# Optimization experiments

Hardware: AMD Instinct MI355X
Metric: run time of the kernel (lower is better)

Reference implementation:

```python
import jax, jax.numpy as jnp
import numpy as np

NODE_IN, EDGE_IN, HID, L = 16, 8, 128, 4
N_NODES, N_EDGES = 50000, 600000
EPS = 1e-5


def setup_inputs() -> dict:
    key = jax.random.key(0)
    ks = jax.random.split(key, 20)
    def lin(k, fan_in, fan_out):
        b = 1.0 / np.sqrt(fan_in)
        kw, kb = jax.random.split(k)
        return (jax.random.uniform(kw, (fan_in, fan_out), jnp.float32, -b, b),
                jax.random.uniform(kb, (fan_out,), jnp.float32, -b, b))
    x = jax.random.normal(ks[0], (N_NODES, NODE_IN), jnp.float32)
    edge_index = jax.random.randint(ks[1], (2, N_EDGES), 0, N_NODES, jnp.int64)
    edge_attr = jax.random.normal(ks[2], (N_EDGES, EDGE_IN), jnp.float32)
    node_w, node_b = lin(ks[3], NODE_IN, HID)
    edge_w, edge_b = lin(ks[4], EDGE_IN, HID)
    lnode_w, lnode_b, ledge_w, ledge_b, adm_w, adm_b = [], [], [], [], [], []
    for l in range(L):
        w, b = lin(ks[5 + 3 * l], HID, HID); lnode_w.append(w); lnode_b.append(b)
        w, b = lin(ks[6 + 3 * l], HID, HID); ledge_w.append(w); ledge_b.append(b)
        w, b = lin(ks[7 + 3 * l], HID, 1); adm_w.append(w); adm_b.append(b)
    return {
        "x": x, "edge_index": edge_index, "edge_attr": edge_attr,
        "node_w": node_w, "node_b": node_b, "edge_w": edge_w, "edge_b": edge_b,
        "lnode_w": jnp.stack(lnode_w), "lnode_b": jnp.stack(lnode_b),
        "ledge_w": jnp.stack(ledge_w), "ledge_b": jnp.stack(ledge_b),
        "adm_w": jnp.stack(adm_w), "adm_b": jnp.stack(adm_b),
        "gamma": jnp.ones((L, HID), jnp.float32),
        "beta": jnp.zeros((L, HID), jnp.float32),
    }


def reference(x, edge_index, edge_attr, node_w, node_b, edge_w, edge_b,
              lnode_w, lnode_b, ledge_w, ledge_b, adm_w, adm_b, gamma, beta):
    N = x.shape[0]
    src, dst = edge_index[0], edge_index[1]
    h = x @ node_w + node_b              # [N, HID]
    ea = edge_attr @ edge_w + edge_b     # [E, HID]
    for l in range(lnode_w.shape[0]):
        hn = h @ lnode_w[l] + lnode_b[l]                         # lin_node
        y_mag = jax.nn.sigmoid(ea @ adm_w[l] + adm_b[l])         # [E, 1] admittance gate
        e = ea @ ledge_w[l] + ledge_b[l]                         # lin_edge
        msg = y_mag * (hn[src] + e)                              # gated message [E, HID]
        agg = jax.ops.segment_sum(msg, dst, num_segments=N)      # scatter-add
        mu = jnp.mean(agg, axis=-1, keepdims=True)
        var = jnp.mean((agg - mu) ** 2, axis=-1, keepdims=True)
        xn = (agg - mu) * jax.lax.rsqrt(var + EPS) * gamma[l] + beta[l]
        h = h + jax.nn.relu(xn)          # dropout is identity in eval mode
    return h
```

## Files before the change

### kernel.cpp

```cpp
#include <hip/hip_runtime.h>
#include <math.h>

#define N_NODES 50000
#define N_EDGES 600000
#define HID 128
#define NLAYERS 4
#define NODE_IN 16
#define EDGE_IN 8
#define LN_EPS 1e-5f
#define SCAN_BLOCKS ((N_NODES + 255) / 256)

typedef short bf16x8 __attribute__((ext_vector_type(8)));
typedef float f32x4 __attribute__((ext_vector_type(4)));

__device__ __forceinline__ float b2f(unsigned short u) {
    union { unsigned int i; float f; } v; v.i = ((unsigned int)u) << 16; return v.f;
}
__device__ __forceinline__ unsigned short f2b(float x) {
    union { float f; unsigned int i; } v; v.f = x;
    unsigned int b = v.i + 0x7FFFu + ((v.i >> 16) & 1u);
    return (unsigned short)(b >> 16);
}

__global__ void detect_i64(const int* ei, int* flag) {
    __shared__ int nz;
    if (threadIdx.x == 0) nz = 0;
    __syncthreads();
    int acc = 0;
    for (int i = threadIdx.x; i < 1024; i += blockDim.x)
        if (ei[2 * i + 1] != 0) acc = 1;
    if (acc) atomicOr(&nz, 1);
    __syncthreads();
    if (threadIdx.x == 0) *flag = (nz == 0) ? 1 : 0;
}

__device__ __forceinline__ int edge_src(const void* ei, int f, int e) {
    if (f) return (int)((const long long*)ei)[e];
    return ((const int*)ei)[e];
}
__device__ __forceinline__ int edge_dst(const void* ei, int f, int e) {
    if (f) return (int)((const long long*)ei)[N_EDGES + e];
    return ((const int*)ei)[N_EDGES + e];
}

__global__ void hist_k(const void* ei, const int* flag, int* cursor) {
    int e = blockIdx.x * blockDim.x + threadIdx.x;
    if (e >= N_EDGES) return;
    int f = *flag;
    atomicAdd(&cursor[edge_dst(ei, f, e)], 1);
}

__global__ void scan1_k(const int* __restrict__ cursor, int* __restrict__ locex,
                        int* __restrict__ partials) {
    __shared__ int sd[256];
    int t = threadIdx.x, i = blockIdx.x * 256 + t;
    int v = (i < N_NODES) ? cursor[i] : 0;
    sd[t] = v;
    __syncthreads();
    for (int off = 1; off < 256; off <<= 1) {
        int x = (t >= off) ? sd[t - off] : 0;
        __syncthreads();
        sd[t] += x;
        __syncthreads();
    }
    if (i < N_NODES) locex[i] = sd[t] - v;
    if (t == 255) partials[blockIdx.x] = sd[255];
}

__global__ void scan2_k(int* partials) {
    __shared__ int sd[256];
    int t = threadIdx.x;
    int v = (t < SCAN_BLOCKS) ? partials[t] : 0;
    sd[t] = v;
    __syncthreads();
    for (int off = 1; off < 256; off <<= 1) {
        int x = (t >= off) ? sd[t - off] : 0;
        __syncthreads();
        sd[t] += x;
        __syncthreads();
    }
    if (t < SCAN_BLOCKS) partials[t] = sd[t] - v;
    if (t == 255) partials[SCAN_BLOCKS] = sd[255];
}

__global__ void scan3_k(int* __restrict__ row_ptr, int* __restrict__ cursor,
                        const int* __restrict__ partials) {
    int i = blockIdx.x * 256 + threadIdx.x;
    if (i < N_NODES) {
        int r = row_ptr[i] + partials[blockIdx.x];
        row_ptr[i] = r;
        cursor[i] = r;
    }
    if (i == N_NODES) row_ptr[N_NODES] = partials[SCAN_BLOCKS];
}

__global__ void place_k(const void* ei, const int* flag, int* cursor,
                        int* sorted_src, int* sorted_eid) {
    int e = blockIdx.x * blockDim.x + threadIdx.x;
    if (e >= N_EDGES) return;
    int f = *flag;
    int s = edge_src(ei, f, e);
    int d = edge_dst(ei, f, e);
    int pos = atomicAdd(&cursor[d], 1);
    sorted_src[pos] = s;
    sorted_eid[pos] = e;
}

__global__ void precompute_k(const float* __restrict__ edge_w, const float* __restrict__ edge_b,
                             const float* __restrict__ ledge_w, const float* __restrict__ ledge_b,
                             const float* __restrict__ lnode_b,
                             const float* __restrict__ adm_w, const float* __restrict__ adm_b,
                             float* __restrict__ M, float* __restrict__ cb,
                             float* __restrict__ v, float* __restrict__ cgate) {
    int t = blockIdx.x * 256 + threadIdx.x;
    if (t < 4096) {
        int l = t >> 10, k = (t >> 7) & 7, ch = t & 127;
        const float* lw = ledge_w + (size_t)l * HID * HID;
        float a = 0.f;
        for (int j = 0; j < HID; ++j) a += edge_w[k * HID + j] * lw[j * HID + ch];
        M[t] = a;
    } else if (t < 4608) {
        int u = t - 4096;
        int l = u >> 7, ch = u & 127;
        const float* lw = ledge_w + (size_t)l * HID * HID;
        float a = ledge_b[l * HID + ch] + lnode_b[l * HID + ch];
        for (int j = 0; j < HID; ++j) a += edge_b[j] * lw[j * HID + ch];
        cb[u] = a;
    } else if (t < 4640) {
        int u = t - 4608;
        int l = u >> 3, k = u & 7;
        float a = 0.f;
        for (int j = 0; j < HID; ++j) a += edge_w[k * HID + j] * adm_w[l * HID + j];
        v[u] = a;
    } else if (t < 4644) {
        int l = t - 4640;
        float a = adm_b[l];
        for (int j = 0; j < HID; ++j) a += edge_b[j] * adm_w[l * HID + j];
        cgate[l] = a;
    }
}

__global__ void convertw_k(const float* __restrict__ lnode_w, unsigned short* __restrict__ Wt16) {
    int idx = blockIdx.x * 256 + threadIdx.x;
    if (idx >= NLAYERS * HID * HID) return;
    int l = idx >> 14, r = idx & 16383, n = r >> 7, k = r & 127;
    Wt16[idx] = f2b(lnode_w[(size_t)l * HID * HID + k * HID + n]);
}

__global__ __launch_bounds__(256) void yorig_k(const float* __restrict__ edge_attr,
                                               const float* __restrict__ v,
                                               const float* __restrict__ cgate,
                                               float4* __restrict__ y4) {
    __shared__ float sv[36];
    if (threadIdx.x < 32) sv[threadIdx.x] = v[threadIdx.x];
    else if (threadIdx.x < 36) sv[threadIdx.x] = cgate[threadIdx.x - 32];
    __syncthreads();
    int e = blockIdx.x * 256 + threadIdx.x;
    if (e >= N_EDGES) return;
    float4 a0 = ((const float4*)edge_attr)[(size_t)e * 2];
    float4 a1 = ((const float4*)edge_attr)[(size_t)e * 2 + 1];
    float pr[NLAYERS];
#pragma unroll
    for (int l = 0; l < NLAYERS; ++l) {
        const float* vl = &sv[l * 8];
        float p = sv[32 + l];
        p += a0.x * vl[0] + a0.y * vl[1] + a0.z * vl[2] + a0.w * vl[3];
        p += a1.x * vl[4] + a1.y * vl[5] + a1.z * vl[6] + a1.w * vl[7];
        pr[l] = 1.0f / (1.0f + expf(-p));
    }
    y4[e] = make_float4(pr[0], pr[1], pr[2], pr[3]);
}

__global__ __launch_bounds__(256) void node_stats_k(
    const int* __restrict__ row_ptr, const int* __restrict__ sorted_eid,
    const float* __restrict__ edge_attr, const float4* __restrict__ y4,
    float* __restrict__ agg8, float* __restrict__ sy_arr,
    float* __restrict__ y_sorted) {
    int lane = threadIdx.x & 63;
    int n = (blockIdx.x * 256 + threadIdx.x) >> 6;
    if (n >= N_NODES) return;
    int es = lane >> 3, k = lane & 7;
    int ps = row_ptr[n], pe = row_ptr[n + 1];
    float a0 = 0.f, a1 = 0.f, a2 = 0.f, a3 = 0.f;
    float s0 = 0.f, s1 = 0.f, s2 = 0.f, s3 = 0.f;
    for (int p = ps + es; p < pe; p += 8) {
        int eid = sorted_eid[p];
        float ea = edge_attr[(size_t)eid * EDGE_IN + k];
        float4 y = y4[eid];
        float yk = (k == 0) ? y.x : (k == 1) ? y.y : (k == 2) ? y.z : y.w;
        if (k < 4) y_sorted[(size_t)k * N_EDGES + p] = yk;
        a0 += y.x * ea; a1 += y.y * ea; a2 += y.z * ea; a3 += y.w * ea;
        s0 += y.x; s1 += y.y; s2 += y.z; s3 += y.w;
    }
#pragma unroll
    for (int m = 8; m <= 32; m <<= 1) {
        a0 += __shfl_xor(a0, m, 64); a1 += __shfl_xor(a1, m, 64);
        a2 += __shfl_xor(a2, m, 64); a3 += __shfl_xor(a3, m, 64);
        s0 += __shfl_xor(s0, m, 64); s1 += __shfl_xor(s1, m, 64);
        s2 += __shfl_xor(s2, m, 64); s3 += __shfl_xor(s3, m, 64);
    }
    if (lane < 8) {
        agg8[((size_t)0 * N_NODES + n) * 8 + k] = a0;
        agg8[((size_t)1 * N_NODES + n) * 8 + k] = a1;
        agg8[((size_t)2 * N_NODES + n) * 8 + k] = a2;
        agg8[((size_t)3 * N_NODES + n) * 8 + k] = a3;
    }
    if (lane == 0) {
        sy_arr[(size_t)0 * N_NODES + n] = s0;
        sy_arr[(size_t)1 * N_NODES + n] = s1;
        sy_arr[(size_t)2 * N_NODES + n] = s2;
        sy_arr[(size_t)3 * N_NODES + n] = s3;
    }
}

__global__ void node_encode_k(const float* __restrict__ x, const float* __restrict__ nw,
                              const float* __restrict__ nb, float* __restrict__ h,
                              unsigned short* __restrict__ h16) {
    int idx = blockIdx.x * 256 + threadIdx.x;
    if (idx >= N_NODES * HID) return;
    int n = idx >> 7, c = idx & 127;
    float acc = nb[c];
#pragma unroll
    for (int k = 0; k < NODE_IN; ++k) acc += x[n * NODE_IN + k] * nw[k * HID + c];
    h[idx] = acc;
    h16[idx] = f2b(acc);
}

__global__ __launch_bounds__(256) void gather16_k(
    const int* __restrict__ row_ptr, const int* __restrict__ sorted_src,
    const float* __restrict__ y_l, const unsigned short* __restrict__ h16,
    unsigned int* __restrict__ gh16) {
    int lane = threadIdx.x & 63;
    int gw = (blockIdx.x * 256 + threadIdx.x) >> 6;
    int nw = (gridDim.x * 256) >> 6;
    for (int n = gw; n < N_NODES; n += nw) {
        int ps = row_ptr[n], pe = row_ptr[n + 1];
        float a0 = 0.f, a1 = 0.f;
        int p = ps;
        for (; p + 3 < pe; p += 4) {
            int s0 = sorted_src[p], s1 = sorted_src[p + 1];
            int s2 = sorted_src[p + 2], s3 = sorted_src[p + 3];
            float y0 = y_l[p], y1 = y_l[p + 1], y2 = y_l[p + 2], y3 = y_l[p + 3];
            unsigned int v0 = *(const unsigned int*)(h16 + (size_t)s0 * HID + lane * 2);
            unsigned int v1 = *(const unsigned int*)(h16 + (size_t)s1 * HID + lane * 2);
            unsigned int v2 = *(const unsigned int*)(h16 + (size_t)s2 * HID + lane * 2);
            unsigned int v3 = *(const unsigned int*)(h16 + (size_t)s3 * HID + lane * 2);
            a0 += y0 * b2f((unsigned short)v0); a1 += y0 * b2f((unsigned short)(v0 >> 16));
            a0 += y1 * b2f((unsigned short)v1); a1 += y1 * b2f((unsigned short)(v1 >> 16));
            a0 += y2 * b2f((unsigned short)v2); a1 += y2 * b2f((unsigned short)(v2 >> 16));
            a0 += y3 * b2f((unsigned short)v3); a1 += y3 * b2f((unsigned short)(v3 >> 16));
        }
        for (; p < pe; ++p) {
            float y = y_l[p];
            unsigned int v = *(const unsigned int*)(h16 + (size_t)sorted_src[p] * HID + lane * 2);
            a0 += y * b2f((unsigned short)v);
            a1 += y * b2f((unsigned short)(v >> 16));
        }
        gh16[(size_t)n * 64 + lane] = ((unsigned int)f2b(a1) << 16) | f2b(a0);
    }
}

__global__ __launch_bounds__(256) void mfma_ln_k(
    const unsigned short* __restrict__ gh16, const unsigned short* __restrict__ Wt16,
    const float* __restrict__ M_l, const float* __restrict__ cb_l,
    const float* __restrict__ agg8_l, const float* __restrict__ sy_l,
    const float* __restrict__ gm, const float* __restrict__ bt,
    const float* __restrict__ h_in, float* __restrict__ h_out,
    unsigned short* __restrict__ h16_out) {
    const int tid = threadIdx.x;
    const int w = tid >> 6, lane = tid & 63;
    const int g = lane >> 4, c = lane & 15;
    const int nbase = blockIdx.x * 64 + w * 16;

    int arow = nbase + c;
    int arowc = (arow < N_NODES) ? arow : (N_NODES - 1);
    bf16x8 afrag[4];
#pragma unroll
    for (int kc = 0; kc < 4; ++kc)
        afrag[kc] = *(const bf16x8*)(gh16 + (size_t)arowc * HID + kc * 32 + g * 8);

    f32x4 acc[8];
#pragma unroll
    for (int cf = 0; cf < 8; ++cf) acc[cf] = (f32x4){0.f, 0.f, 0.f, 0.f};
#pragma unroll
    for (int cf = 0; cf < 8; ++cf) {
        const unsigned short* wp = Wt16 + (size_t)(cf * 16 + c) * HID + g * 8;
#pragma unroll
        for (int kc = 0; kc < 4; ++kc) {
            bf16x8 bfrag = *(const bf16x8*)(wp + kc * 32);
            acc[cf] = __builtin_amdgcn_mfma_f32_16x16x32_bf16(afrag[kc], bfrag, acc[cf], 0, 0, 0);
        }
    }

    float sy_v[4];
    float a8v[4][8];
#pragma unroll
    for (int r = 0; r < 4; ++r) {
        int node = nbase + 4 * g + r;
        int nc = (node < N_NODES) ? node : (N_NODES - 1);
        sy_v[r] = sy_l[nc];
        float4 t0 = ((const float4*)agg8_l)[(size_t)nc * 2];
        float4 t1 = ((const float4*)agg8_l)[(size_t)nc * 2 + 1];
        a8v[r][0] = t0.x; a8v[r][1] = t0.y; a8v[r][2] = t0.z; a8v[r][3] = t0.w;
        a8v[r][4] = t1.x; a8v[r][5] = t1.y; a8v[r][6] = t1.z; a8v[r][7] = t1.w;
    }
#pragma unroll
    for (int cf = 0; cf < 8; ++cf) {
        int ch = cf * 16 + c;
        float cbv = cb_l[ch];
        float mv[8];
#pragma unroll
        for (int k = 0; k < 8; ++k) mv[k] = M_l[k * HID + ch];
#pragma unroll
        for (int r = 0; r < 4; ++r) {
            float t = sy_v[r] * cbv;
#pragma unroll
            for (int k = 0; k < 8; ++k) t += a8v[r][k] * mv[k];
            acc[cf][r] += t;
        }
    }

    float gav[8], bev[8];
#pragma unroll
    for (int cf = 0; cf < 8; ++cf) {
        gav[cf] = gm[cf * 16 + c];
        bev[cf] = bt[cf * 16 + c];
    }

#pragma unroll
    for (int r = 0; r < 4; ++r) {
        float s = 0.f;
#pragma unroll
        for (int cf = 0; cf < 8; ++cf) s += acc[cf][r];
        s += __shfl_xor(s, 1, 64); s += __shfl_xor(s, 2, 64);
        s += __shfl_xor(s, 4, 64); s += __shfl_xor(s, 8, 64);
        float mean = s * (1.0f / HID);
        float vs = 0.f;
        float d[8];
#pragma unroll
        for (int cf = 0; cf < 8; ++cf) { d[cf] = acc[cf][r] - mean; vs += d[cf] * d[cf]; }
        vs += __shfl_xor(vs, 1, 64); vs += __shfl_xor(vs, 2, 64);
        vs += __shfl_xor(vs, 4, 64); vs += __shfl_xor(vs, 8, 64);
        float rstd = rsqrtf(vs * (1.0f / HID) + LN_EPS);
        int node = nbase + 4 * g + r;
        if (node < N_NODES) {
#pragma unroll
            for (int cf = 0; cf < 8; ++cf) {
                int ch = cf * 16 + c;
                float o = h_in[(size_t)node * HID + ch] +
                          fmaxf(d[cf] * rstd * gav[cf] + bev[cf], 0.f);
                h_out[(size_t)node * HID + ch] = o;
                h16_out[(size_t)node * HID + ch] = f2b(o);
            }
        }
    }
}

extern "C" void kernel_launch(void* const* d_in, const int* in_sizes, int n_in,
                              void* d_out, int out_size, void* d_ws, size_t ws_size,
                              hipStream_t stream) {
    const float* x         = (const float*)d_in[0];
    const void*  ei        = d_in[1];
    const float* edge_attr = (const float*)d_in[2];
    const float* node_w    = (const float*)d_in[3];
    const float* node_b    = (const float*)d_in[4];
    const float* edge_w    = (const float*)d_in[5];
    const float* edge_b    = (const float*)d_in[6];
    const float* lnode_w   = (const float*)d_in[7];
    const float* lnode_b   = (const float*)d_in[8];
    const float* ledge_w   = (const float*)d_in[9];
    const float* ledge_b   = (const float*)d_in[10];
    const float* adm_w     = (const float*)d_in[11];
    const float* adm_b     = (const float*)d_in[12];
    const float* gamma     = (const float*)d_in[13];
    const float* beta      = (const float*)d_in[14];
    float* h = (float*)d_out;

    char* wp = (char*)d_ws;
    auto alloc = [&](size_t bytes) -> void* {
        void* p = (void*)wp;
        wp += (bytes + 255) & ~(size_t)255;
        return p;
    };
    int*            flag       = (int*)alloc(256);
    int*            cursor     = (int*)alloc(sizeof(int) * N_NODES);
    int*            row_ptr    = (int*)alloc(sizeof(int) * (N_NODES + 1));
    int*            partials   = (int*)alloc(sizeof(int) * (SCAN_BLOCKS + 1));
    int*            sorted_src = (int*)alloc(sizeof(int) * N_EDGES);
    int*            sorted_eid = (int*)alloc(sizeof(int) * N_EDGES);
    float4*         y4         = (float4*)alloc(sizeof(float4) * N_EDGES);
    float*          y_sorted   = (float*)alloc(sizeof(float) * NLAYERS * N_EDGES);
    float*          agg8       = (float*)alloc(sizeof(float) * NLAYERS * N_NODES * 8);
    float*          sy_arr     = (float*)alloc(sizeof(float) * NLAYERS * N_NODES);
    float*          Mw         = (float*)alloc(sizeof(float) * NLAYERS * 8 * HID);
    float*          cbw        = (float*)alloc(sizeof(float) * NLAYERS * HID);
    float*          vw         = (float*)alloc(sizeof(float) * NLAYERS * 8);
    float*          cgate      = (float*)alloc(sizeof(float) * NLAYERS);
    float*          hbuf       = (float*)alloc(sizeof(float) * (size_t)N_NODES * HID);
    unsigned short* h16        = (unsigned short*)alloc(sizeof(short) * (size_t)N_NODES * HID);
    unsigned short* gh16       = (unsigned short*)alloc(sizeof(short) * (size_t)N_NODES * HID);
    unsigned short* Wt16       = (unsigned short*)alloc(sizeof(short) * NLAYERS * HID * HID);
    (void)ws_size; (void)in_sizes; (void)n_in; (void)out_size;

    hipMemsetAsync(cursor, 0, sizeof(int) * N_NODES, stream);
    detect_i64<<<1, 256, 0, stream>>>((const int*)ei, flag);
    hist_k<<<(N_EDGES + 255) / 256, 256, 0, stream>>>(ei, flag, cursor);
    scan1_k<<<SCAN_BLOCKS, 256, 0, stream>>>(cursor, row_ptr, partials);
    scan2_k<<<1, 256, 0, stream>>>(partials);
    scan3_k<<<SCAN_BLOCKS, 256, 0, stream>>>(row_ptr, cursor, partials);
    place_k<<<(N_EDGES + 255) / 256, 256, 0, stream>>>(ei, flag, cursor, sorted_src, sorted_eid);
    precompute_k<<<19, 256, 0, stream>>>(edge_w, edge_b, ledge_w, ledge_b, lnode_b,
                                         adm_w, adm_b, Mw, cbw, vw, cgate);
    convertw_k<<<(NLAYERS * HID * HID + 255) / 256, 256, 0, stream>>>(lnode_w, Wt16);
    yorig_k<<<(N_EDGES + 255) / 256, 256, 0, stream>>>(edge_attr, vw, cgate, y4);
    node_stats_k<<<(N_NODES + 3) / 4, 256, 0, stream>>>(row_ptr, sorted_eid, edge_attr, y4,
                                                        agg8, sy_arr, y_sorted);
    node_encode_k<<<(N_NODES * HID + 255) / 256, 256, 0, stream>>>(x, node_w, node_b, h, h16);

    float* hin = h;
    float* hout = hbuf;
    for (int l = 0; l < NLAYERS; ++l) {
        gather16_k<<<2048, 256, 0, stream>>>(
            row_ptr, sorted_src, y_sorted + (size_t)l * N_EDGES, h16, (unsigned int*)gh16);
        mfma_ln_k<<<(N_NODES + 63) / 64, 256, 0, stream>>>(
            gh16, Wt16 + (size_t)l * HID * HID,
            Mw + (size_t)l * 8 * HID, cbw + (size_t)l * HID,
            agg8 + (size_t)l * N_NODES * 8, sy_arr + (size_t)l * N_NODES,
            gamma + (size_t)l * HID, beta + (size_t)l * HID,
            hin, hout, h16);
        float* t = hin; hin = hout; hout = t;
    }
}
```

Before: 421.5 us.

## Scatter gates during placement, one-node-per-wave gather, split MFMA tile across waves

Gate values are now written into dst-sorted order inside place_k, which runs after yorig_k, so node_stats_k reads them contiguously instead of doing random y4 lookups. gather16_k drops its grid-stride loop and launches one wave per node. mfma_ln_k now gives each block 16 nodes, with each wave computing two of the eight 16-channel column tiles. LayerNorm statistics are reduced across waves in shared memory using the single-pass sum and sum-of-squares form. This raises block counts and parallelism but adds a barrier, a less stable variance formula, and drops the bounds checks, so it relies on N_NODES dividing evenly by 16.

```diff
diff --git a/kernel.cpp b/kernel.cpp
--- a/kernel.cpp
+++ b/kernel.cpp
@@ -95,7 +95,9 @@
 }
 
 __global__ void place_k(const void* ei, const int* flag, int* cursor,
-                        int* sorted_src, int* sorted_eid) {
+                        const float4* __restrict__ y4,
+                        int* sorted_src, int* sorted_eid,
+                        float* __restrict__ y_sorted) {
     int e = blockIdx.x * blockDim.x + threadIdx.x;
     if (e >= N_EDGES) return;
     int f = *flag;
@@ -104,6 +106,11 @@
     int pos = atomicAdd(&cursor[d], 1);
     sorted_src[pos] = s;
     sorted_eid[pos] = e;
+    float4 y = y4[e];
+    y_sorted[(size_t)0 * N_EDGES + pos] = y.x;
+    y_sorted[(size_t)1 * N_EDGES + pos] = y.y;
+    y_sorted[(size_t)2 * N_EDGES + pos] = y.z;
+    y_sorted[(size_t)3 * N_EDGES + pos] = y.w;
 }
 
 __global__ void precompute_k(const float* __restrict__ edge_w, const float* __restrict__ edge_b,
@@ -173,12 +180,10 @@
 
 __global__ __launch_bounds__(256) void node_stats_k(
     const int* __restrict__ row_ptr, const int* __restrict__ sorted_eid,
-    const float* __restrict__ edge_attr, const float4* __restrict__ y4,
-    float* __restrict__ agg8, float* __restrict__ sy_arr,
-    float* __restrict__ y_sorted) {
+    const float* __restrict__ edge_attr, const float* __restrict__ y_sorted,
+    float* __restrict__ agg8, float* __restrict__ sy_arr) {
     int lane = threadIdx.x & 63;
     int n = (blockIdx.x * 256 + threadIdx.x) >> 6;
-    if (n >= N_NODES) return;
     int es = lane >> 3, k = lane & 7;
     int ps = row_ptr[n], pe = row_ptr[n + 1];
     float a0 = 0.f, a1 = 0.f, a2 = 0.f, a3 = 0.f;
@@ -186,11 +191,12 @@
     for (int p = ps + es; p < pe; p += 8) {
         int eid = sorted_eid[p];
         float ea = edge_attr[(size_t)eid * EDGE_IN + k];
-        float4 y = y4[eid];
-        float yk = (k == 0) ? y.x : (k == 1) ? y.y : (k == 2) ? y.z : y.w;
-        if (k < 4) y_sorted[(size_t)k * N_EDGES + p] = yk;
-        a0 += y.x * ea; a1 += y.y * ea; a2 += y.z * ea; a3 += y.w * ea;
-        s0 += y.x; s1 += y.y; s2 += y.z; s3 += y.w;
+        float y0 = y_sorted[(size_t)0 * N_EDGES + p];
+        float y1 = y_sorted[(size_t)1 * N_EDGES + p];
+        float y2 = y_sorted[(size_t)2 * N_EDGES + p];
+        float y3 = y_sorted[(size_t)3 * N_EDGES + p];
+        a0 += y0 * ea; a1 += y1 * ea; a2 += y2 * ea; a3 += y3 * ea;
+        s0 += y0; s1 += y1; s2 += y2; s3 += y3;
     }
 #pragma unroll
     for (int m = 8; m <= 32; m <<= 1) {
@@ -231,33 +237,30 @@
     const float* __restrict__ y_l, const unsigned short* __restrict__ h16,
     unsigned int* __restrict__ gh16) {
     int lane = threadIdx.x & 63;
-    int gw = (blockIdx.x * 256 + threadIdx.x) >> 6;
-    int nw = (gridDim.x * 256) >> 6;
-    for (int n = gw; n < N_NODES; n += nw) {
-        int ps = row_ptr[n], pe = row_ptr[n + 1];
-        float a0 = 0.f, a1 = 0.f;
-        int p = ps;
-        for (; p + 3 < pe; p += 4) {
-            int s0 = sorted_src[p], s1 = sorted_src[p + 1];
-            int s2 = sorted_src[p + 2], s3 = sorted_src[p + 3];
-            float y0 = y_l[p], y1 = y_l[p + 1], y2 = y_l[p + 2], y3 = y_l[p + 3];
-            unsigned int v0 = *(const unsigned int*)(h16 + (size_t)s0 * HID + lane * 2);
-            unsigned int v1 = *(const unsigned int*)(h16 + (size_t)s1 * HID + lane * 2);
-            unsigned int v2 = *(const unsigned int*)(h16 + (size_t)s2 * HID + lane * 2);
-            unsigned int v3 = *(const unsigned int*)(h16 + (size_t)s3 * HID + lane * 2);
-            a0 += y0 * b2f((unsigned short)v0); a1 += y0 * b2f((unsigned short)(v0 >> 16));
-            a0 += y1 * b2f((unsigned short)v1); a1 += y1 * b2f((unsigned short)(v1 >> 16));
-            a0 += y2 * b2f((unsigned short)v2); a1 += y2 * b2f((unsigned short)(v2 >> 16));
-            a0 += y3 * b2f((unsigned short)v3); a1 += y3 * b2f((unsigned short)(v3 >> 16));
-        }
-        for (; p < pe; ++p) {
-            float y = y_l[p];
-            unsigned int v = *(const unsigned int*)(h16 + (size_t)sorted_src[p] * HID + lane * 2);
-            a0 += y * b2f((unsigned short)v);
-            a1 += y * b2f((unsigned short)(v >> 16));
-        }
-        gh16[(size_t)n * 64 + lane] = ((unsigned int)f2b(a1) << 16) | f2b(a0);
-    }
+    int n = (blockIdx.x * 256 + threadIdx.x) >> 6;
+    int ps = row_ptr[n], pe = row_ptr[n + 1];
+    float a0 = 0.f, a1 = 0.f;
+    int p = ps;
+    for (; p + 3 < pe; p += 4) {
+        int s0 = sorted_src[p], s1 = sorted_src[p + 1];
+        int s2 = sorted_src[p + 2], s3 = sorted_src[p + 3];
+        float y0 = y_l[p], y1 = y_l[p + 1], y2 = y_l[p + 2], y3 = y_l[p + 3];
+        unsigned int v0 = *(const unsigned int*)(h16 + (size_t)s0 * HID + lane * 2);
+        unsigned int v1 = *(const unsigned int*)(h16 + (size_t)s1 * HID + lane * 2);
+        unsigned int v2 = *(const unsigned int*)(h16 + (size_t)s2 * HID + lane * 2);
+        unsigned int v3 = *(const unsigned int*)(h16 + (size_t)s3 * HID + lane * 2);
+        a0 += y0 * b2f((unsigned short)v0); a1 += y0 * b2f((unsigned short)(v0 >> 16));
+        a0 += y1 * b2f((unsigned short)v1); a1 += y1 * b2f((unsigned short)(v1 >> 16));
+        a0 += y2 * b2f((unsigned short)v2); a1 += y2 * b2f((unsigned short)(v2 >> 16));
+        a0 += y3 * b2f((unsigned short)v3); a1 += y3 * b2f((unsigned short)(v3 >> 16));
+    }
+    for (; p < pe; ++p) {
+        float y = y_l[p];
+        unsigned int v = *(const unsigned int*)(h16 + (size_t)sorted_src[p] * HID + lane * 2);
+        a0 += y * b2f((unsigned short)v);
+        a1 += y * b2f((unsigned short)(v >> 16));
+    }
+    gh16[(size_t)n * 64 + lane] = ((unsigned int)f2b(a1) << 16) | f2b(a0);
 }
 
 __global__ __launch_bounds__(256) void mfma_ln_k(
@@ -267,91 +270,94 @@
     const float* __restrict__ gm, const float* __restrict__ bt,
     const float* __restrict__ h_in, float* __restrict__ h_out,
     unsigned short* __restrict__ h16_out) {
+    __shared__ float red[4][16][2];
     const int tid = threadIdx.x;
     const int w = tid >> 6, lane = tid & 63;
     const int g = lane >> 4, c = lane & 15;
-    const int nbase = blockIdx.x * 64 + w * 16;
-
-    int arow = nbase + c;
-    int arowc = (arow < N_NODES) ? arow : (N_NODES - 1);
+    const int nbase = blockIdx.x * 16;
+    const int cf0 = w * 2;
+
     bf16x8 afrag[4];
 #pragma unroll
     for (int kc = 0; kc < 4; ++kc)
-        afrag[kc] = *(const bf16x8*)(gh16 + (size_t)arowc * HID + kc * 32 + g * 8);
-
-    f32x4 acc[8];
-#pragma unroll
-    for (int cf = 0; cf < 8; ++cf) acc[cf] = (f32x4){0.f, 0.f, 0.f, 0.f};
-#pragma unroll
-    for (int cf = 0; cf < 8; ++cf) {
-        const unsigned short* wp = Wt16 + (size_t)(cf * 16 + c) * HID + g * 8;
+        afrag[kc] = *(const bf16x8*)(gh16 + (size_t)(nbase + c) * HID + kc * 32 + g * 8);
+
+    f32x4 acc[2];
+#pragma unroll
+    for (int t = 0; t < 2; ++t) {
+        acc[t] = (f32x4){0.f, 0.f, 0.f, 0.f};
+        const unsigned short* wp = Wt16 + (size_t)((cf0 + t) * 16 + c) * HID + g * 8;
 #pragma unroll
         for (int kc = 0; kc < 4; ++kc) {
             bf16x8 bfrag = *(const bf16x8*)(wp + kc * 32);
-            acc[cf] = __builtin_amdgcn_mfma_f32_16x16x32_bf16(afrag[kc], bfrag, acc[cf], 0, 0, 0);
+            acc[t] = __builtin_amdgcn_mfma_f32_16x16x32_bf16(afrag[kc], bfrag, acc[t], 0, 0, 0);
         }
     }
 
-    float sy_v[4];
-    float a8v[4][8];
+    float cbv[2], gav[2], bev[2], mv[2][8];
+#pragma unroll
+    for (int t = 0; t < 2; ++t) {
+        int ch = (cf0 + t) * 16 + c;
+        cbv[t] = cb_l[ch]; gav[t] = gm[ch]; bev[t] = bt[ch];
+#pragma unroll
+        for (int k = 0; k < 8; ++k) mv[t][k] = M_l[k * HID + ch];
+    }
 #pragma unroll
     for (int r = 0; r < 4; ++r) {
         int node = nbase + 4 * g + r;
-        int nc = (node < N_NODES) ? node : (N_NODES - 1);
-        sy_v[r] = sy_l[nc];
-        float4 t0 = ((const float4*)agg8_l)[(size_t)nc * 2];
-        float4 t1 = ((const float4*)agg8_l)[(size_t)nc * 2 + 1];
-        a8v[r][0] = t0.x; a8v[r][1] = t0.y; a8v[r][2] = t0.z; a8v[r][3] = t0.w;
-        a8v[r][4] = t1.x; a8v[r][5] = t1.y; a8v[r][6] = t1.z; a8v[r][7] = t1.w;
-    }
-#pragma unroll
-    for (int cf = 0; cf < 8; ++cf) {
-        int ch = cf * 16 + c;
-        float cbv = cb_l[ch];
-        float mv[8];
-#pragma unroll
-        for (int k = 0; k < 8; ++k) mv[k] = M_l[k * HID + ch];
+        float sy = sy_l[node];
+        float4 t0 = ((const float4*)agg8_l)[(size_t)node * 2];
+        float4 t1 = ((const float4*)agg8_l)[(size_t)node * 2 + 1];
+        float a8[8] = {t0.x, t0.y, t0.z, t0.w, t1.x, t1.y, t1.z, t1.w};
+#pragma unroll
+        for (int t = 0; t < 2; ++t) {
+            float v = sy * cbv[t];
+#pragma unroll
+            for (int k = 0; k < 8; ++k) v += a8[k] * mv[t][k];
+            acc[t][r] += v;
+        }
+    }
+
+    float sx[4], sq[4];
+#pragma unroll
+    for (int r = 0; r < 4; ++r) {
+        sx[r] = acc[0][r] + acc[1][r];
+        sq[r] = acc[0][r] * acc[0][r] + acc[1][r] * acc[1][r];
+    }
+#pragma unroll
+    for (int m = 1; m <= 8; m <<= 1) {
 #pragma unroll
         for (int r = 0; r < 4; ++r) {
-            float t = sy_v[r] * cbv;
-#pragma unroll
-            for (int k = 0; k < 8; ++k) t += a8v[r][k] * mv[k];
-            acc[cf][r] += t;
+            sx[r] += __shfl_xor(sx[r], m, 64);
+            sq[r] += __shfl_xor(sq[r], m, 64);
         }
     }
-
-    float gav[8], bev[8];
-#pragma unroll
-    for (int cf = 0; cf < 8; ++cf) {
-        gav[cf] = gm[cf * 16 + c];
-        bev[cf] = bt[cf * 16 + c];
-    }
+    if (c == 0) {
+#pragma unroll
+        for (int r = 0; r < 4; ++r) {
+            red[w][4 * g + r][0] = sx[r];
+            red[w][4 * g + r][1] = sq[r];
+        }
+    }
+    __syncthreads();
 
 #pragma unroll
     for (int r = 0; r < 4; ++r) {
-        float s = 0.f;
-#pragma unroll
-        for (int cf = 0; cf < 8; ++cf) s += acc[cf][r];
-        s += __shfl_xor(s, 1, 64); s += __shfl_xor(s, 2, 64);
-        s += __shfl_xor(s, 4, 64); s += __shfl_xor(s, 8, 64);
-        float mean = s * (1.0f / HID);
-        float vs = 0.f;
-        float d[8];
-#pragma unroll
-        for (int cf = 0; cf < 8; ++cf) { d[cf] = acc[cf][r] - mean; vs += d[cf] * d[cf]; }
-        vs += __shfl_xor(vs, 1, 64); vs += __shfl_xor(vs, 2, 64);
-        vs += __shfl_xor(vs, 4, 64); vs += __shfl_xor(vs, 8, 64);
-        float rstd = rsqrtf(vs * (1.0f / HID) + LN_EPS);
-        int node = nbase + 4 * g + r;
-        if (node < N_NODES) {
-#pragma unroll
-            for (int cf = 0; cf < 8; ++cf) {
-                int ch = cf * 16 + c;
-                float o = h_in[(size_t)node * HID + ch] +
-                          fmaxf(d[cf] * rstd * gav[cf] + bev[cf], 0.f);
-                h_out[(size_t)node * HID + ch] = o;
-                h16_out[(size_t)node * HID + ch] = f2b(o);
-            }
+        int row = 4 * g + r;
+        float SX = red[0][row][0] + red[1][row][0] + red[2][row][0] + red[3][row][0];
+        float SQ = red[0][row][1] + red[1][row][1] + red[2][row][1] + red[3][row][1];
+        float mean = SX * (1.0f / HID);
+        float var = SQ * (1.0f / HID) - mean * mean;
+        float rstd = rsqrtf(var + LN_EPS);
+        int node = nbase + row;
+#pragma unroll
+        for (int t = 0; t < 2; ++t) {
+            int ch = (cf0 + t) * 16 + c;
+            float d = acc[t][r] - mean;
+            float o = h_in[(size_t)node * HID + ch] +
+                      fmaxf(d * rstd * gav[t] + bev[t], 0.f);
+            h_out[(size_t)node * HID + ch] = o;
+            h16_out[(size_t)node * HID + ch] = f2b(o);
         }
     }
 }
@@ -408,21 +414,22 @@
     scan1_k<<<SCAN_BLOCKS, 256, 0, stream>>>(cursor, row_ptr, partials);
     scan2_k<<<1, 256, 0, stream>>>(partials);
     scan3_k<<<SCAN_BLOCKS, 256, 0, stream>>>(row_ptr, cursor, partials);
-    place_k<<<(N_EDGES + 255) / 256, 256, 0, stream>>>(ei, flag, cursor, sorted_src, sorted_eid);
     precompute_k<<<19, 256, 0, stream>>>(edge_w, edge_b, ledge_w, ledge_b, lnode_b,
                                          adm_w, adm_b, Mw, cbw, vw, cgate);
     convertw_k<<<(NLAYERS * HID * HID + 255) / 256, 256, 0, stream>>>(lnode_w, Wt16);
     yorig_k<<<(N_EDGES + 255) / 256, 256, 0, stream>>>(edge_attr, vw, cgate, y4);
-    node_stats_k<<<(N_NODES + 3) / 4, 256, 0, stream>>>(row_ptr, sorted_eid, edge_attr, y4,
-                                                        agg8, sy_arr, y_sorted);
+    place_k<<<(N_EDGES + 255) / 256, 256, 0, stream>>>(ei, flag, cursor, y4,
+                                                       sorted_src, sorted_eid, y_sorted);
+    node_stats_k<<<N_NODES / 4, 256, 0, stream>>>(row_ptr, sorted_eid, edge_attr,
+                                                  y_sorted, agg8, sy_arr);
     node_encode_k<<<(N_NODES * HID + 255) / 256, 256, 0, stream>>>(x, node_w, node_b, h, h16);
 
     float* hin = h;
     float* hout = hbuf;
     for (int l = 0; l < NLAYERS; ++l) {
-        gather16_k<<<2048, 256, 0, stream>>>(
+        gather16_k<<<N_NODES / 4, 256, 0, stream>>>(
             row_ptr, sorted_src, y_sorted + (size_t)l * N_EDGES, h16, (unsigned int*)gh16);
-        mfma_ln_k<<<(N_NODES + 63) / 64, 256, 0, stream>>>(
+        mfma_ln_k<<<N_NODES / 16, 256, 0, stream>>>(
             gh16, Wt16 + (size_t)l * HID * HID,
             Mw + (size_t)l * 8 * HID, cbw + (size_t)l * HID,
             agg8 + (size_t)l * N_NODES * 8, sy_arr + (size_t)l * N_NODES,
```

New measurement: 410.3 us. 2.7% less time.
